# Performance work log

Measured on AMD Instinct MI355X. Metric: run time of the kernel, lower is better.

Reference implementation:

```python
import jax, jax.numpy as jnp
import numpy as np
from jax import lax

BN_EPS = 1e-5


def _conv_bn_relu(x, W, b, gamma, beta):
    # x: [B, Cin, N]; W: [Cout, Cin]; 1x1 conv == channel GEMM
    y = jnp.einsum('oc,bcn->bon', W, x) + b[None, :, None]
    mean = jnp.mean(y, axis=(0, 2), keepdims=True)
    var = jnp.mean((y - mean) ** 2, axis=(0, 2), keepdims=True)  # biased, torch BN train mode
    y = gamma[None, :, None] * (y - mean) / jnp.sqrt(var + BN_EPS) + beta[None, :, None]
    return jax.nn.relu(y)


def setup_inputs() -> dict:
    key = jax.random.key(0)
    ks = jax.random.split(key, 8)
    B, N1, N2, C1, C2 = 16, 4096, 1024, 128, 256
    Cin, H = C1 + C2, 256  # MLP dims [384, 256, 256]
    inp = {
        'centroids1': jax.random.normal(ks[0], (B, 3, N1), jnp.float32),
        'centroids2': jax.random.normal(ks[1], (B, 3, N2), jnp.float32),
        'features1': jax.random.normal(ks[2], (B, C1, N1), jnp.float32),
        'features2': jax.random.normal(ks[3], (B, C2, N2), jnp.float32),
        'W1': jax.random.normal(ks[4], (H, Cin), jnp.float32) / np.sqrt(Cin),
        'b1': jnp.zeros((H,), jnp.float32),
        'g1': jnp.ones((H,), jnp.float32),
        'be1': jnp.zeros((H,), jnp.float32),
        'W2': jax.random.normal(ks[5], (H, H), jnp.float32) / np.sqrt(H),
        'b2': jnp.zeros((H,), jnp.float32),
        'g2': jnp.ones((H,), jnp.float32),
        'be2': jnp.zeros((H,), jnp.float32),
    }
    return inp


def reference(centroids1, centroids2, features1, features2,
              W1, b1, g1, be1, W2, b2, g2, be2):
    c1 = centroids1.transpose(0, 2, 1)  # [B, N1, 3]
    c2 = centroids2.transpose(0, 2, 1)  # [B, N2, 3]
    f2 = features2.transpose(0, 2, 1)   # [B, N2, C2]

    # pairwise squared distances [B, N1, N2]
    d = (jnp.sum(c1 ** 2, -1)[:, :, None] + jnp.sum(c2 ** 2, -1)[:, None, :]
         - 2.0 * jnp.einsum('bnd,bmd->bnm', c1, c2))

    # 3 nearest neighbors (smallest distances)
    neg_top, idx = lax.top_k(-d, 3)            # idx: [B, N1, 3]
    dist3 = -neg_top
    recip = 1.0 / (dist3 + 1e-8)
    weight = recip / jnp.sum(recip, axis=2, keepdims=True)  # [B, N1, 3]

    gathered = jax.vmap(lambda f, i: f[i])(f2, idx)         # [B, N1, 3, C2]
    interp = jnp.sum(gathered * weight[..., None], axis=2)  # [B, N1, C2]

    feats = jnp.concatenate((features1.transpose(0, 2, 1), interp), axis=-1)  # [B, N1, C1+C2]
    x = feats.transpose(0, 2, 1)  # [B, C1+C2, N1]
    x = _conv_bn_relu(x, W1, b1, g1, be1)
    x = _conv_bn_relu(x, W2, b2, g2, be2)
    return x  # [B, 256, N1]
```

## Files before the change

### kernel.cpp

```cpp
#include <hip/hip_runtime.h>
#include <math.h>

#define N1 4096
#define N2 1024
#define C1 128
#define C2 256
#define CIN 384
#define H 256
#define BATCH 16
#define BN_EPS 1e-5f

typedef __attribute__((ext_vector_type(8))) short bf16x8;
typedef __attribute__((ext_vector_type(4))) float f32x4;

__device__ inline float bf2f(short s) {
    union { unsigned u; float f; } x;
    x.u = ((unsigned)(unsigned short)s) << 16;
    return x.f;
}
__device__ inline short f2bf(float f) {
    union { float f; unsigned u; } x; x.f = f;
    unsigned r = x.u + 0x7fffu + ((x.u >> 16) & 1u);
    return (short)(r >> 16);
}

typedef const __attribute__((address_space(1))) unsigned int guint;
typedef __attribute__((address_space(3))) unsigned int luint;
__device__ inline void gll16(const void* g, void* l) {
    __builtin_amdgcn_global_load_lds((guint*)g, (luint*)l, 16, 0, 0);
}

__global__ __launch_bounds__(512)
void knn_kernel(const float* __restrict__ c1, const float* __restrict__ c2,
                float4* __restrict__ pk) {
    __shared__ __align__(16) float4 sc[N2];
    __shared__ float md[64 * 25];
    __shared__ int   mi[64 * 25];
    const int b = blockIdx.y;
    const float* c2b = c2 + (size_t)b * 3 * N2;
    for (int j = threadIdx.x; j < N2; j += 512) {
        float xx = c2b[j], yy = c2b[N2 + j], zz = c2b[2 * N2 + j];
        sc[j] = make_float4(-2.f * xx, -2.f * yy, -2.f * zz, xx * xx + yy * yy + zz * zz);
    }
    __syncthreads();

    const int t = threadIdx.x;
    const int q = t & 63;
    const int oct = t >> 6;
    const int n = blockIdx.x * 64 + q;
    const float* c1b = c1 + (size_t)b * 3 * N1;
    const float x = c1b[n], y = c1b[N1 + n], z = c1b[2 * N1 + n];

    float d0 = 3.4e38f, d1 = 3.4e38f, d2 = 3.4e38f;
    int i0 = 0, i1 = 0, i2 = 0;
    const int j0 = oct * 128;
    #pragma unroll 8
    for (int jj = 0; jj < 128; ++jj) {
        const int j = j0 + jj;
        float4 cc = sc[j];
        float d = fmaf(x, cc.x, fmaf(y, cc.y, fmaf(z, cc.z, cc.w)));
        bool c0v = d < d0, c1v = d < d1, c2v = d < d2;
        i2 = c1v ? i1 : (c2v ? j : i2);
        i1 = c0v ? i0 : (c1v ? j : i1);
        i0 = c0v ? j  : i0;
        d2 = __builtin_amdgcn_fmed3f(d1, d2, d);
        d1 = __builtin_amdgcn_fmed3f(d0, d1, d);
        d0 = fminf(d0, d);
    }
    const int mb = q * 25 + oct * 3;
    md[mb + 0] = d0; md[mb + 1] = d1; md[mb + 2] = d2;
    mi[mb + 0] = i0; mi[mb + 1] = i1; mi[mb + 2] = i2;
    __syncthreads();

    if (t < 64) {
        float e0 = 3.4e38f, e1 = 3.4e38f, e2 = 3.4e38f;
        int a0 = 0, a1 = 0, a2 = 0;
        #pragma unroll
        for (int r = 0; r < 24; ++r) {
            const int rr = t * 25 + r;
            float d = md[rr]; int j = mi[rr];
            bool c0 = d < e0, c1v = d < e1, c2v = d < e2;
            e2 = c1v ? e1 : (c2v ? d : e2);  a2 = c1v ? a1 : (c2v ? j : a2);
            e1 = c0 ? e0 : (c1v ? d : e1);   a1 = c0 ? a0 : (c1v ? j : a1);
            e0 = c0 ? d  : e0;               a0 = c0 ? j  : a0;
        }
        const float s1 = x * x + y * y + z * z;
        float r0 = 1.0f / (e0 + s1 + 1e-8f);
        float r1 = 1.0f / (e1 + s1 + 1e-8f);
        float r2 = 1.0f / (e2 + s1 + 1e-8f);
        float rs = r0 + r1 + r2;
        unsigned pack = (unsigned)a0 | ((unsigned)a1 << 10) | ((unsigned)a2 << 20);
        pk[(size_t)b * N1 + n] = make_float4(__uint_as_float(pack), r0 / rs, r1 / rs, r2 / rs);
    }
}

__global__ __launch_bounds__(256)
void prep_w(const float* __restrict__ W, short* __restrict__ Wsw, int K) {
    const int nkb = K >> 3;
    const int id = blockIdx.x * 256 + threadIdx.x;
    if (id >= 256 * nkb) return;
    const int m = id / nkb, kb = id % nkb;
    const float* src = W + (size_t)m * K + kb * 8;
    bf16x8 v;
    #pragma unroll
    for (int j = 0; j < 8; ++j) v[j] = f2bf(src[j]);
    *(bf16x8*)(Wsw + ((size_t)kb * 256 + m) * 8) = v;
}

__global__ __launch_bounds__(256)
void transpose_f2(const float* __restrict__ f2, short* __restrict__ f2t) {
    __shared__ float st[32][33];
    const int j0 = blockIdx.x * 32, c0 = blockIdx.y * 32, b = blockIdx.z;
    const int t = threadIdx.x;
    {
        const int cc = t >> 3, jj = (t & 7) * 4;
        const float* src = f2 + ((size_t)b * C2 + c0 + cc) * N2 + j0 + jj;
        float4 v = *(const float4*)src;
        st[cc][jj + 0] = v.x; st[cc][jj + 1] = v.y;
        st[cc][jj + 2] = v.z; st[cc][jj + 3] = v.w;
    }
    __syncthreads();
    {
        const int j = t >> 3, cb = (t & 7) * 4;
        short4 v = { f2bf(st[cb + 0][j]), f2bf(st[cb + 1][j]),
                     f2bf(st[cb + 2][j]), f2bf(st[cb + 3][j]) };
        *(short4*)(f2t + ((size_t)b * N2 + j0 + j) * C2 + c0 + cb) = v;
    }
}

template<int NT, bool BN>
__global__ __launch_bounds__(256)
void gemm_kernel(const short* __restrict__ Wsw,
                 const float* __restrict__ f1, const short* __restrict__ Bkc,
                 const short* __restrict__ f2t, const float4* __restrict__ pk,
                 const float* __restrict__ scale, const float* __restrict__ shift,
                 short* __restrict__ Ykc, float2* __restrict__ P) {
    constexpr bool M0 = (NT == 12);

    __shared__ __align__(16) short B_lds[4 * NT][64][8];
    __shared__ float sc_s[256], sh_s[256];

    const int t = threadIdx.x;
    const int blk = blockIdx.x;
    const int b = blk >> 6, nt = blk & 63;
    const int n0 = nt * 64;

    const int lane = t & 63, wv = t >> 6;
    const int wm = wv;
    const int l16 = lane & 15, lq = lane >> 4;

    if (BN) { sc_s[t] = scale[t]; sh_s[t] = shift[t]; }

    if (M0) {
        const int col = t & 63;
        const int kq  = t >> 6;
        float4 pv = pk[(size_t)b * N1 + n0 + col];
        unsigned u = __float_as_uint(pv.x);
        const short* rr0 = f2t + ((size_t)b * N2 + (u & 1023u)) * C2;
        const short* rr1 = f2t + ((size_t)b * N2 + ((u >> 10) & 1023u)) * C2;
        const short* rr2 = f2t + ((size_t)b * N2 + ((u >> 20) & 1023u)) * C2;
        #pragma unroll
        for (int i = 0; i < 8; ++i) {
            const int kbl = i * 4 + kq;
            bf16x8 g0 = *(const bf16x8*)(rr0 + kbl * 8);
            bf16x8 g1 = *(const bf16x8*)(rr1 + kbl * 8);
            bf16x8 g2 = *(const bf16x8*)(rr2 + kbl * 8);
            bf16x8 o;
            #pragma unroll
            for (int e = 0; e < 8; ++e)
                o[e] = f2bf(fmaf(pv.w, bf2f(g2[e]), fmaf(pv.z, bf2f(g1[e]), pv.y * bf2f(g0[e]))));
            *(bf16x8*)&B_lds[16 + kbl][col][0] = o;
        }
        const float* f1b = f1 + (size_t)b * C1 * N1;
        const int kbt = t >> 4, nq = (t & 15) * 4;
        float4 fv[8];
        #pragma unroll
        for (int e = 0; e < 8; ++e)
            fv[e] = *(const float4*)(f1b + (size_t)(kbt * 8 + e) * N1 + n0 + nq);
        #pragma unroll
        for (int j = 0; j < 4; ++j) {
            bf16x8 pw;
            pw[0] = f2bf(j == 0 ? fv[0].x : j == 1 ? fv[0].y : j == 2 ? fv[0].z : fv[0].w);
            pw[1] = f2bf(j == 0 ? fv[1].x : j == 1 ? fv[1].y : j == 2 ? fv[1].z : fv[1].w);
            pw[2] = f2bf(j == 0 ? fv[2].x : j == 1 ? fv[2].y : j == 2 ? fv[2].z : fv[2].w);
            pw[3] = f2bf(j == 0 ? fv[3].x : j == 1 ? fv[3].y : j == 2 ? fv[3].z : fv[3].w);
            pw[4] = f2bf(j == 0 ? fv[4].x : j == 1 ? fv[4].y : j == 2 ? fv[4].z : fv[4].w);
            pw[5] = f2bf(j == 0 ? fv[5].x : j == 1 ? fv[5].y : j == 2 ? fv[5].z : fv[5].w);
            pw[6] = f2bf(j == 0 ? fv[6].x : j == 1 ? fv[6].y : j == 2 ? fv[6].z : fv[6].w);
            pw[7] = f2bf(j == 0 ? fv[7].x : j == 1 ? fv[7].y : j == 2 ? fv[7].z : fv[7].w);
            *(bf16x8*)&B_lds[kbt][nq + j][0] = pw;
        }
    } else {
        const short* Bb = Bkc + (size_t)b * 32 * N1 * 8;
        #pragma unroll
        for (int i = 0; i < 8; ++i) {
            const int u = wv * 8 + i;
            const short* g = Bb + ((size_t)u * N1 + n0 + lane) * 8;
            gll16(g, &B_lds[u][0][0]);
        }
    }
    __syncthreads();

    f32x4 acc[4][4];
    #pragma unroll
    for (int i = 0; i < 4; ++i)
        #pragma unroll
        for (int j = 0; j < 4; ++j)
            acc[i][j] = (f32x4){0.f, 0.f, 0.f, 0.f};

    #pragma unroll
    for (int s = 0; s < NT; ++s) {
        bf16x8 a[4], bb4[4];
        const short* ap = Wsw + ((size_t)(s * 4 + lq) * 256 + wm * 64 + l16) * 8;
        #pragma unroll
        for (int f = 0; f < 4; ++f)
            a[f] = *(const bf16x8*)(ap + (size_t)f * 16 * 8);
        if (BN) {
            const int k0 = s * 32 + lq * 8;
            float sck[8], shk[8];
            #pragma unroll
            for (int e = 0; e < 8; ++e) { sck[e] = sc_s[k0 + e]; shk[e] = sh_s[k0 + e]; }
            #pragma unroll
            for (int f = 0; f < 4; ++f) {
                bf16x8 raw = *(const bf16x8*)&B_lds[s * 4 + lq][f * 16 + l16][0];
                #pragma unroll
                for (int e = 0; e < 8; ++e)
                    bb4[f][e] = f2bf(fmaxf(fmaf(bf2f(raw[e]), sck[e], shk[e]), 0.f));
            }
        } else {
            #pragma unroll
            for (int f = 0; f < 4; ++f)
                bb4[f] = *(const bf16x8*)&B_lds[s * 4 + lq][f * 16 + l16][0];
        }
        #pragma unroll
        for (int i = 0; i < 4; ++i)
            #pragma unroll
            for (int j = 0; j < 4; ++j)
                acc[i][j] = __builtin_amdgcn_mfma_f32_16x16x32_bf16(a[i], bb4[j], acc[i][j], 0, 0, 0);
    }

    short* Yb = Ykc + (size_t)b * 32 * N1 * 8;
    #pragma unroll
    for (int i = 0; i < 4; ++i) {
        const int kb = wm * 8 + i * 2 + (lq >> 1);
        const int kr0 = (lq & 1) * 4;
        #pragma unroll
        for (int j = 0; j < 4; ++j) {
            const int n = n0 + j * 16 + l16;
            short4 v = { f2bf(acc[i][j][0]), f2bf(acc[i][j][1]),
                         f2bf(acc[i][j][2]), f2bf(acc[i][j][3]) };
            *(short4*)(Yb + ((size_t)kb * N1 + n) * 8 + kr0) = v;
        }
    }

    #pragma unroll
    for (int i = 0; i < 4; ++i) {
        #pragma unroll
        for (int r = 0; r < 4; ++r) {
            float s = 0.f, qq = 0.f;
            #pragma unroll
            for (int j = 0; j < 4; ++j) {
                float xv = acc[i][j][r];
                s += xv; qq += xv * xv;
            }
            #pragma unroll
            for (int msk = 1; msk < 16; msk <<= 1) {
                s  += __shfl_xor(s, msk);
                qq += __shfl_xor(qq, msk);
            }
            if (l16 == 0) {
                const int c = wm * 64 + i * 16 + lq * 4 + r;
                P[(size_t)c * 1024 + blk] = make_float2(s, qq);
            }
        }
    }
}

__global__ __launch_bounds__(256)
void bn_reduce(const float2* __restrict__ P, const float* __restrict__ g,
               const float* __restrict__ be, float* __restrict__ scale,
               float* __restrict__ shift) {
    const int c = blockIdx.x, t = threadIdx.x;
    float s = 0.f, q = 0.f;
    #pragma unroll
    for (int r = 0; r < 4; ++r) {
        float2 v = P[(size_t)c * 1024 + r * 256 + t];
        s += v.x; q += v.y;
    }
    __shared__ float ss[256], sq[256];
    ss[t] = s; sq[t] = q;
    __syncthreads();
    for (int o = 128; o > 0; o >>= 1) {
        if (t < o) { ss[t] += ss[t + o]; sq[t] += sq[t + o]; }
        __syncthreads();
    }
    if (t == 0) {
        const float inv = 1.0f / (float)(BATCH * N1);
        float mean = ss[0] * inv;
        float var  = sq[0] * inv - mean * mean;
        float sc = g[c] / sqrtf(var + BN_EPS);
        scale[c] = sc;
        shift[c] = be[c] - mean * sc;
    }
}

__global__ __launch_bounds__(256)
void final_bn_relu(const short* __restrict__ y2kc, const float* __restrict__ scale,
                   const float* __restrict__ shift, float* __restrict__ out) {
    const int t = threadIdx.x;
    const int n0 = blockIdx.x * 1024 + t * 4;
    const int kb = blockIdx.y, b = blockIdx.z;
    const short* src = y2kc + ((size_t)(b * 32 + kb) * N1 + n0) * 8;
    bf16x8 v0 = *(const bf16x8*)(src);
    bf16x8 v1 = *(const bf16x8*)(src + 8);
    bf16x8 v2 = *(const bf16x8*)(src + 16);
    bf16x8 v3 = *(const bf16x8*)(src + 24);
    #pragma unroll
    for (int e = 0; e < 8; ++e) {
        const float sc = scale[kb * 8 + e], sh = shift[kb * 8 + e];
        float4 o;
        o.x = fmaxf(fmaf(bf2f(v0[e]), sc, sh), 0.f);
        o.y = fmaxf(fmaf(bf2f(v1[e]), sc, sh), 0.f);
        o.z = fmaxf(fmaf(bf2f(v2[e]), sc, sh), 0.f);
        o.w = fmaxf(fmaf(bf2f(v3[e]), sc, sh), 0.f);
        *(float4*)(out + ((size_t)(b * 256 + kb * 8 + e) * N1) + n0) = o;
    }
}

extern "C" void kernel_launch(void* const* d_in, const int* in_sizes, int n_in,
                              void* d_out, int out_size, void* d_ws, size_t ws_size,
                              hipStream_t stream) {
    const float* c1  = (const float*)d_in[0];
    const float* c2  = (const float*)d_in[1];
    const float* f1  = (const float*)d_in[2];
    const float* f2  = (const float*)d_in[3];
    const float* W1  = (const float*)d_in[4];
    const float* g1  = (const float*)d_in[6];
    const float* be1 = (const float*)d_in[7];
    const float* W2  = (const float*)d_in[8];
    const float* g2  = (const float*)d_in[10];
    const float* be2 = (const float*)d_in[11];
    float* out = (float*)d_out;

    char* ws = (char*)d_ws;
    short*  y1kc = (short*)ws;
    short*  f2t  = (short*)(ws + (32u << 20));
    short*  y2kc = (short*)(ws + (32u << 20));
    short*  W1s  = (short*)(ws + (64u << 20));
    short*  W2s  = (short*)(ws + (64u << 20) + (256u << 10));
    float4* pk   = (float4*)(ws + (64u << 20) + (512u << 10));
    float2* P    = (float2*)(ws + (64u << 20) + (1536u << 10));
    float* scale1 = (float*)(ws + (64u << 20) + (3584u << 10));
    float* shift1 = scale1 + 256;
    float* scale2 = shift1 + 256;
    float* shift2 = scale2 + 256;

    prep_w<<<48, 256, 0, stream>>>(W1, W1s, CIN);
    prep_w<<<32, 256, 0, stream>>>(W2, W2s, H);
    transpose_f2<<<dim3(N2 / 32, C2 / 32, BATCH), 256, 0, stream>>>(f2, f2t);
    knn_kernel<<<dim3(N1 / 64, BATCH), 512, 0, stream>>>(c1, c2, pk);

    gemm_kernel<12, false><<<1024, 256, 0, stream>>>(
        W1s, f1, nullptr, f2t, pk, nullptr, nullptr, y1kc, P);
    bn_reduce<<<256, 256, 0, stream>>>(P, g1, be1, scale1, shift1);

    gemm_kernel<8, true><<<1024, 256, 0, stream>>>(
        W2s, nullptr, y1kc, nullptr, nullptr, scale1, shift1, y2kc, P);
    bn_reduce<<<256, 256, 0, stream>>>(P, g2, be2, scale2, shift2);

    final_bn_relu<<<dim3(N1 / 1024, 32, BATCH), 256, 0, stream>>>(y2kc, scale2, shift2, out);
}
```

Measured before the change: 140.2 us.

## Split GEMMs into persistent multi-tile kernels with double-buffered LDS staging

The templated GEMM is split into two specialised kernels. Each block now loops over several column tiles and stages the next tile into a second LDS buffer while it computes the current one. GEMM1 moves to 32-column tiles on a 768-block grid with uneven 3/2 tile counts, which means more partial BN sums (2048 per channel) and a templated bn_reduce. GEMM2 runs 512 blocks with two tiles each, using async global-to-LDS loads and a partial vmcnt wait. Together these aim to hide gather and load latency and to cut per-block overhead, at the cost of a different workspace layout and less MFMA work per wave in GEMM1.

Result: slower. 160.0 us (+14.1%).

```diff
diff --git a/kernel.cpp b/kernel.cpp
--- a/kernel.cpp
+++ b/kernel.cpp
@@ -128,40 +128,33 @@
     }
 }
 
-template<int NT, bool BN>
-__global__ __launch_bounds__(256)
-void gemm_kernel(const short* __restrict__ Wsw,
-                 const float* __restrict__ f1, const short* __restrict__ Bkc,
-                 const short* __restrict__ f2t, const float4* __restrict__ pk,
-                 const float* __restrict__ scale, const float* __restrict__ shift,
-                 short* __restrict__ Ykc, float2* __restrict__ P) {
-    constexpr bool M0 = (NT == 12);
-
-    __shared__ __align__(16) short B_lds[4 * NT][64][8];
-    __shared__ float sc_s[256], sh_s[256];
+__global__ __launch_bounds__(256)
+void gemm1_kernel(const short* __restrict__ Wsw,
+                  const float* __restrict__ f1, const short* __restrict__ f2t,
+                  const float4* __restrict__ pk,
+                  short* __restrict__ Ykc, float2* __restrict__ P) {
+    __shared__ __align__(16) short B_lds[2][48][32][8];
 
     const int t = threadIdx.x;
     const int blk = blockIdx.x;
-    const int b = blk >> 6, nt = blk & 63;
-    const int n0 = nt * 64;
+    const int ntile = (blk < 512) ? 3 : 2;
 
     const int lane = t & 63, wv = t >> 6;
     const int wm = wv;
     const int l16 = lane & 15, lq = lane >> 4;
 
-    if (BN) { sc_s[t] = scale[t]; sh_s[t] = shift[t]; }
-
-    if (M0) {
-        const int col = t & 63;
-        const int kq  = t >> 6;
-        float4 pv = pk[(size_t)b * N1 + n0 + col];
+    auto stage = [&](int tile, int bufi) {
+        const int bb = tile >> 7;
+        const int n0t = (tile & 127) * 32;
+        const int col = t & 31, kq = t >> 5;
+        float4 pv = pk[(size_t)bb * N1 + n0t + col];
         unsigned u = __float_as_uint(pv.x);
-        const short* rr0 = f2t + ((size_t)b * N2 + (u & 1023u)) * C2;
-        const short* rr1 = f2t + ((size_t)b * N2 + ((u >> 10) & 1023u)) * C2;
-        const short* rr2 = f2t + ((size_t)b * N2 + ((u >> 20) & 1023u)) * C2;
-        #pragma unroll
-        for (int i = 0; i < 8; ++i) {
-            const int kbl = i * 4 + kq;
+        const short* rr0 = f2t + ((size_t)bb * N2 + (u & 1023u)) * C2;
+        const short* rr1 = f2t + ((size_t)bb * N2 + ((u >> 10) & 1023u)) * C2;
+        const short* rr2 = f2t + ((size_t)bb * N2 + ((u >> 20) & 1023u)) * C2;
+        #pragma unroll
+        for (int i = 0; i < 4; ++i) {
+            const int kbl = i * 8 + kq;
             bf16x8 g0 = *(const bf16x8*)(rr0 + kbl * 8);
             bf16x8 g1 = *(const bf16x8*)(rr1 + kbl * 8);
             bf16x8 g2 = *(const bf16x8*)(rr2 + kbl * 8);
@@ -169,113 +162,199 @@
             #pragma unroll
             for (int e = 0; e < 8; ++e)
                 o[e] = f2bf(fmaf(pv.w, bf2f(g2[e]), fmaf(pv.z, bf2f(g1[e]), pv.y * bf2f(g0[e]))));
-            *(bf16x8*)&B_lds[16 + kbl][col][0] = o;
-        }
-        const float* f1b = f1 + (size_t)b * C1 * N1;
-        const int kbt = t >> 4, nq = (t & 15) * 4;
-        float4 fv[8];
-        #pragma unroll
-        for (int e = 0; e < 8; ++e)
-            fv[e] = *(const float4*)(f1b + (size_t)(kbt * 8 + e) * N1 + n0 + nq);
-        #pragma unroll
-        for (int j = 0; j < 4; ++j) {
-            bf16x8 pw;
-            pw[0] = f2bf(j == 0 ? fv[0].x : j == 1 ? fv[0].y : j == 2 ? fv[0].z : fv[0].w);
-            pw[1] = f2bf(j == 0 ? fv[1].x : j == 1 ? fv[1].y : j == 2 ? fv[1].z : fv[1].w);
-            pw[2] = f2bf(j == 0 ? fv[2].x : j == 1 ? fv[2].y : j == 2 ? fv[2].z : fv[2].w);
-            pw[3] = f2bf(j == 0 ? fv[3].x : j == 1 ? fv[3].y : j == 2 ? fv[3].z : fv[3].w);
-            pw[4] = f2bf(j == 0 ? fv[4].x : j == 1 ? fv[4].y : j == 2 ? fv[4].z : fv[4].w);
-            pw[5] = f2bf(j == 0 ? fv[5].x : j == 1 ? fv[5].y : j == 2 ? fv[5].z : fv[5].w);
-            pw[6] = f2bf(j == 0 ? fv[6].x : j == 1 ? fv[6].y : j == 2 ? fv[6].z : fv[6].w);
-            pw[7] = f2bf(j == 0 ? fv[7].x : j == 1 ? fv[7].y : j == 2 ? fv[7].z : fv[7].w);
-            *(bf16x8*)&B_lds[kbt][nq + j][0] = pw;
-        }
-    } else {
-        const short* Bb = Bkc + (size_t)b * 32 * N1 * 8;
+            *(bf16x8*)&B_lds[bufi][16 + kbl][col][0] = o;
+        }
+        const float* f1b = f1 + (size_t)bb * C1 * N1;
+        const int kbt = t >> 4, col2 = (t & 15) * 2;
+        bf16x8 p0, p1;
+        #pragma unroll
+        for (int e = 0; e < 8; ++e) {
+            float2 v = *(const float2*)(f1b + (size_t)(kbt * 8 + e) * N1 + n0t + col2);
+            p0[e] = f2bf(v.x); p1[e] = f2bf(v.y);
+        }
+        *(bf16x8*)&B_lds[bufi][kbt][col2][0]     = p0;
+        *(bf16x8*)&B_lds[bufi][kbt][col2 + 1][0] = p1;
+    };
+
+    stage(blk, 0);
+    __syncthreads();
+
+    int buf = 0;
+    for (int ti = 0; ti < ntile; ++ti) {
+        const int tile = blk + ti * 768;
+        if (ti + 1 < ntile) stage(blk + (ti + 1) * 768, buf ^ 1);
+
+        f32x4 acc[4][2];
+        #pragma unroll
+        for (int i = 0; i < 4; ++i) {
+            acc[i][0] = (f32x4){0.f, 0.f, 0.f, 0.f};
+            acc[i][1] = (f32x4){0.f, 0.f, 0.f, 0.f};
+        }
+        #pragma unroll
+        for (int s = 0; s < 12; ++s) {
+            bf16x8 a[4], bb4[2];
+            const short* ap = Wsw + ((size_t)(s * 4 + lq) * 256 + wm * 64 + l16) * 8;
+            #pragma unroll
+            for (int f = 0; f < 4; ++f)
+                a[f] = *(const bf16x8*)(ap + (size_t)f * 16 * 8);
+            bb4[0] = *(const bf16x8*)&B_lds[buf][s * 4 + lq][l16][0];
+            bb4[1] = *(const bf16x8*)&B_lds[buf][s * 4 + lq][16 + l16][0];
+            #pragma unroll
+            for (int i = 0; i < 4; ++i) {
+                acc[i][0] = __builtin_amdgcn_mfma_f32_16x16x32_bf16(a[i], bb4[0], acc[i][0], 0, 0, 0);
+                acc[i][1] = __builtin_amdgcn_mfma_f32_16x16x32_bf16(a[i], bb4[1], acc[i][1], 0, 0, 0);
+            }
+        }
+
+        const int bb = tile >> 7;
+        const int n0t = (tile & 127) * 32;
+        short* Yb = Ykc + (size_t)bb * 32 * N1 * 8;
+        #pragma unroll
+        for (int i = 0; i < 4; ++i) {
+            const int kb = wm * 8 + i * 2 + (lq >> 1);
+            const int kr0 = (lq & 1) * 4;
+            #pragma unroll
+            for (int j = 0; j < 2; ++j) {
+                const int n = n0t + j * 16 + l16;
+                short4 v = { f2bf(acc[i][j][0]), f2bf(acc[i][j][1]),
+                             f2bf(acc[i][j][2]), f2bf(acc[i][j][3]) };
+                *(short4*)(Yb + ((size_t)kb * N1 + n) * 8 + kr0) = v;
+            }
+        }
+        #pragma unroll
+        for (int i = 0; i < 4; ++i) {
+            #pragma unroll
+            for (int r = 0; r < 4; ++r) {
+                float s = acc[i][0][r] + acc[i][1][r];
+                float qq = acc[i][0][r] * acc[i][0][r] + acc[i][1][r] * acc[i][1][r];
+                #pragma unroll
+                for (int msk = 1; msk < 16; msk <<= 1) {
+                    s  += __shfl_xor(s, msk);
+                    qq += __shfl_xor(qq, msk);
+                }
+                if (l16 == 0) {
+                    const int c = wm * 64 + i * 16 + lq * 4 + r;
+                    P[(size_t)c * 2048 + tile] = make_float2(s, qq);
+                }
+            }
+        }
+        __syncthreads();
+        buf ^= 1;
+    }
+}
+
+__global__ __launch_bounds__(256)
+void gemm2_kernel(const short* __restrict__ Wsw, const short* __restrict__ y1kc,
+                  const float* __restrict__ scale, const float* __restrict__ shift,
+                  short* __restrict__ Ykc, float2* __restrict__ P) {
+    __shared__ __align__(16) short B_lds[2][32][64][8];
+    __shared__ float sc_s[256], sh_s[256];
+
+    const int t = threadIdx.x;
+    const int blk = blockIdx.x;
+    const int lane = t & 63, wv = t >> 6;
+    const int wm = wv;
+    const int l16 = lane & 15, lq = lane >> 4;
+
+    sc_s[t] = scale[t]; sh_s[t] = shift[t];
+    __syncthreads();
+
+    auto stage = [&](int tile, int bufi) {
+        const int bb = tile >> 6;
+        const int n0t = (tile & 63) * 64;
         #pragma unroll
         for (int i = 0; i < 8; ++i) {
             const int u = wv * 8 + i;
-            const short* g = Bb + ((size_t)u * N1 + n0 + lane) * 8;
-            gll16(g, &B_lds[u][0][0]);
-        }
-    }
-    __syncthreads();
-
-    f32x4 acc[4][4];
+            const short* g = y1kc + (((size_t)bb * 32 + u) * N1 + n0t + lane) * 8;
+            gll16(g, &B_lds[bufi][u][0][0]);
+        }
+    };
+
+    stage(blk, 0);
+    stage(blk + 512, 1);
+
+    asm volatile("s_waitcnt vmcnt(8)" ::: "memory");
+    __builtin_amdgcn_sched_barrier(0);
+    __builtin_amdgcn_s_barrier();
+    __builtin_amdgcn_sched_barrier(0);
+
     #pragma unroll
-    for (int i = 0; i < 4; ++i)
-        #pragma unroll
-        for (int j = 0; j < 4; ++j)
-            acc[i][j] = (f32x4){0.f, 0.f, 0.f, 0.f};
-
-    #pragma unroll
-    for (int s = 0; s < NT; ++s) {
-        bf16x8 a[4], bb4[4];
-        const short* ap = Wsw + ((size_t)(s * 4 + lq) * 256 + wm * 64 + l16) * 8;
-        #pragma unroll
-        for (int f = 0; f < 4; ++f)
-            a[f] = *(const bf16x8*)(ap + (size_t)f * 16 * 8);
-        if (BN) {
+    for (int ti = 0; ti < 2; ++ti) {
+        const int tile = blk + ti * 512;
+        const int bb = tile >> 6;
+        const int n0t = (tile & 63) * 64;
+
+        f32x4 acc[4][4];
+        #pragma unroll
+        for (int i = 0; i < 4; ++i)
+            #pragma unroll
+            for (int j = 0; j < 4; ++j)
+                acc[i][j] = (f32x4){0.f, 0.f, 0.f, 0.f};
+
+        #pragma unroll
+        for (int s = 0; s < 8; ++s) {
+            bf16x8 a[4], bb4[4];
+            const short* ap = Wsw + ((size_t)(s * 4 + lq) * 256 + wm * 64 + l16) * 8;
+            #pragma unroll
+            for (int f = 0; f < 4; ++f)
+                a[f] = *(const bf16x8*)(ap + (size_t)f * 16 * 8);
             const int k0 = s * 32 + lq * 8;
             float sck[8], shk[8];
             #pragma unroll
             for (int e = 0; e < 8; ++e) { sck[e] = sc_s[k0 + e]; shk[e] = sh_s[k0 + e]; }
             #pragma unroll
             for (int f = 0; f < 4; ++f) {
-                bf16x8 raw = *(const bf16x8*)&B_lds[s * 4 + lq][f * 16 + l16][0];
+                bf16x8 raw = *(const bf16x8*)&B_lds[ti][s * 4 + lq][f * 16 + l16][0];
                 #pragma unroll
                 for (int e = 0; e < 8; ++e)
                     bb4[f][e] = f2bf(fmaxf(fmaf(bf2f(raw[e]), sck[e], shk[e]), 0.f));
             }
-        } else {
-            #pragma unroll
-            for (int f = 0; f < 4; ++f)
-                bb4[f] = *(const bf16x8*)&B_lds[s * 4 + lq][f * 16 + l16][0];
-        }
-        #pragma unroll
-        for (int i = 0; i < 4; ++i)
-            #pragma unroll
-            for (int j = 0; j < 4; ++j)
-                acc[i][j] = __builtin_amdgcn_mfma_f32_16x16x32_bf16(a[i], bb4[j], acc[i][j], 0, 0, 0);
-    }
-
-    short* Yb = Ykc + (size_t)b * 32 * N1 * 8;
-    #pragma unroll
-    for (int i = 0; i < 4; ++i) {
-        const int kb = wm * 8 + i * 2 + (lq >> 1);
-        const int kr0 = (lq & 1) * 4;
-        #pragma unroll
-        for (int j = 0; j < 4; ++j) {
-            const int n = n0 + j * 16 + l16;
-            short4 v = { f2bf(acc[i][j][0]), f2bf(acc[i][j][1]),
-                         f2bf(acc[i][j][2]), f2bf(acc[i][j][3]) };
-            *(short4*)(Yb + ((size_t)kb * N1 + n) * 8 + kr0) = v;
-        }
-    }
-
-    #pragma unroll
-    for (int i = 0; i < 4; ++i) {
-        #pragma unroll
-        for (int r = 0; r < 4; ++r) {
-            float s = 0.f, qq = 0.f;
+            #pragma unroll
+            for (int i = 0; i < 4; ++i)
+                #pragma unroll
+                for (int j = 0; j < 4; ++j)
+                    acc[i][j] = __builtin_amdgcn_mfma_f32_16x16x32_bf16(a[i], bb4[j], acc[i][j], 0, 0, 0);
+        }
+
+        short* Yb = Ykc + (size_t)bb * 32 * N1 * 8;
+        #pragma unroll
+        for (int i = 0; i < 4; ++i) {
+            const int kb = wm * 8 + i * 2 + (lq >> 1);
+            const int kr0 = (lq & 1) * 4;
             #pragma unroll
             for (int j = 0; j < 4; ++j) {
-                float xv = acc[i][j][r];
-                s += xv; qq += xv * xv;
-            }
-            #pragma unroll
-            for (int msk = 1; msk < 16; msk <<= 1) {
-                s  += __shfl_xor(s, msk);
-                qq += __shfl_xor(qq, msk);
-            }
-            if (l16 == 0) {
-                const int c = wm * 64 + i * 16 + lq * 4 + r;
-                P[(size_t)c * 1024 + blk] = make_float2(s, qq);
-            }
-        }
-    }
-}
-
+                const int n = n0t + j * 16 + l16;
+                short4 v = { f2bf(acc[i][j][0]), f2bf(acc[i][j][1]),
+                             f2bf(acc[i][j][2]), f2bf(acc[i][j][3]) };
+                *(short4*)(Yb + ((size_t)kb * N1 + n) * 8 + kr0) = v;
+            }
+        }
+        #pragma unroll
+        for (int i = 0; i < 4; ++i) {
+            #pragma unroll
+            for (int r = 0; r < 4; ++r) {
+                float s = 0.f, qq = 0.f;
+                #pragma unroll
+                for (int j = 0; j < 4; ++j) {
+                    float xv = acc[i][j][r];
+                    s += xv; qq += xv * xv;
+                }
+                #pragma unroll
+                for (int msk = 1; msk < 16; msk <<= 1) {
+                    s  += __shfl_xor(s, msk);
+                    qq += __shfl_xor(qq, msk);
+                }
+                if (l16 == 0) {
+                    const int c = wm * 64 + i * 16 + lq * 4 + r;
+                    P[(size_t)c * 1024 + tile] = make_float2(s, qq);
+                }
+            }
+        }
+        if (ti == 0) __syncthreads();
+    }
+}
+
+template<int NP>
 __global__ __launch_bounds__(256)
 void bn_reduce(const float2* __restrict__ P, const float* __restrict__ g,
                const float* __restrict__ be, float* __restrict__ scale,
@@ -283,8 +362,8 @@
     const int c = blockIdx.x, t = threadIdx.x;
     float s = 0.f, q = 0.f;
     #pragma unroll
-    for (int r = 0; r < 4; ++r) {
-        float2 v = P[(size_t)c * 1024 + r * 256 + t];
+    for (int r = 0; r < NP / 256; ++r) {
+        float2 v = P[(size_t)c * NP + r * 256 + t];
         s += v.x; q += v.y;
     }
     __shared__ float ss[256], sq[256];
@@ -345,12 +424,13 @@
     char* ws = (char*)d_ws;
     short*  y1kc = (short*)ws;
     short*  f2t  = (short*)(ws + (32u << 20));
+    float4* pk   = (float4*)(ws + (40u << 20));
+    float2* P1   = (float2*)(ws + (41u << 20));
     short*  y2kc = (short*)(ws + (32u << 20));
     short*  W1s  = (short*)(ws + (64u << 20));
-    short*  W2s  = (short*)(ws + (64u << 20) + (256u << 10));
-    float4* pk   = (float4*)(ws + (64u << 20) + (512u << 10));
-    float2* P    = (float2*)(ws + (64u << 20) + (1536u << 10));
-    float* scale1 = (float*)(ws + (64u << 20) + (3584u << 10));
+    short*  W2s  = (short*)(ws + (64u << 20) + (192u << 10));
+    float2* P2   = (float2*)(ws + (64u << 20) + (320u << 10));
+    float* scale1 = (float*)(ws + (64u << 20) + (320u << 10) + (2u << 20));
     float* shift1 = scale1 + 256;
     float* scale2 = shift1 + 256;
     float* shift2 = scale2 + 256;
@@ -360,13 +440,11 @@
     transpose_f2<<<dim3(N2 / 32, C2 / 32, BATCH), 256, 0, stream>>>(f2, f2t);
     knn_kernel<<<dim3(N1 / 64, BATCH), 512, 0, stream>>>(c1, c2, pk);
 
-    gemm_kernel<12, false><<<1024, 256, 0, stream>>>(
-        W1s, f1, nullptr, f2t, pk, nullptr, nullptr, y1kc, P);
-    bn_reduce<<<256, 256, 0, stream>>>(P, g1, be1, scale1, shift1);
-
-    gemm_kernel<8, true><<<1024, 256, 0, stream>>>(
-        W2s, nullptr, y1kc, nullptr, nullptr, scale1, shift1, y2kc, P);
-    bn_reduce<<<256, 256, 0, stream>>>(P, g2, be2, scale2, shift2);
+    gemm1_kernel<<<768, 256, 0, stream>>>(W1s, f1, f2t, pk, y1kc, P1);
+    bn_reduce<2048><<<256, 256, 0, stream>>>(P1, g1, be1, scale1, shift1);
+
+    gemm2_kernel<<<512, 256, 0, stream>>>(W2s, y1kc, scale1, shift1, y2kc, P2);
+    bn_reduce<1024><<<256, 256, 0, stream>>>(P2, g2, be2, scale2, shift2);
 
     final_bn_relu<<<dim3(N1 / 1024, 32, BATCH), 256, 0, stream>>>(y2kc, scale2, shift2, out);
 }
```
